# Performance work log

Hardware: AMD Instinct MI355X
Metric: run time of the kernel (lower is better)

The kernel has to match this reference:

```python
import jax, jax.numpy as jnp
import numpy as np

B, T, D = 2, 2048, 2048
H, KV, HD = 16, 8, 128
N_REP = H // KV
EPS = 1e-6
ROPE_THETA = 5e6
K_MASK = float(jnp.finfo(jnp.bfloat16).min)


def setup_inputs() -> dict:
    key = jax.random.key(0)
    ks = jax.random.split(key, 8)
    x = jax.random.normal(ks[0], (B, T, D), dtype=jnp.float32)
    wq = jax.random.normal(ks[1], (D, H * HD), dtype=jnp.float32) * 0.02
    wk = jax.random.normal(ks[2], (D, KV * HD), dtype=jnp.float32) * 0.02
    wv = jax.random.normal(ks[3], (D, KV * HD), dtype=jnp.float32) * 0.02
    wo = jax.random.normal(ks[4], (H * HD, D), dtype=jnp.float32) * 0.02
    qn_w = jnp.ones((HD,), dtype=jnp.float32)
    kn_w = jnp.ones((HD,), dtype=jnp.float32)
    # real rotary angles: [T, HD//2] -> broadcast to [B, T, HD//2]
    pos = jnp.arange(T, dtype=jnp.float32)
    inv_freq = 1.0 / (ROPE_THETA ** (jnp.arange(0, HD, 2, dtype=jnp.float32) / HD))
    ang = pos[:, None] * inv_freq[None, :]
    sin = jnp.broadcast_to(jnp.sin(ang)[None], (B, T, HD // 2))
    cos = jnp.broadcast_to(jnp.cos(ang)[None], (B, T, HD // 2))
    # causal mask [B, 1, T, T]
    causal = jnp.tril(jnp.ones((T, T), dtype=jnp.bool_))
    mask = jnp.broadcast_to(causal[None, None], (B, 1, T, T))
    k_cache = jnp.zeros((B, T, KV, HD), dtype=jnp.float32)
    v_cache = jnp.zeros((B, T, KV, HD), dtype=jnp.float32)
    return {"x": x, "wq": wq, "wk": wk, "wv": wv, "wo": wo,
            "qn_w": qn_w, "kn_w": kn_w, "sin": sin, "cos": cos,
            "mask": mask, "k_cache": k_cache, "v_cache": v_cache}


def _rms_norm(h, w):
    h32 = h.astype(jnp.float32)
    rms = jax.lax.rsqrt(jnp.mean(h32 * h32, axis=-1, keepdims=True) + EPS)
    return (h32 * rms * w).astype(h.dtype)


def _apply_rope(x, sin, cos):
    x1, x2 = x[..., : HD // 2], x[..., HD // 2:]
    s, c = sin[:, :, None, :], cos[:, :, None, :]  # [B,T,1,HD/2]
    return jnp.concatenate([x1 * c - x2 * s, x2 * c + x1 * s], axis=-1).astype(x.dtype)


def reference(x, wq, wk, wv, wo, qn_w, kn_w, sin, cos, mask, k_cache, v_cache):
    b, t, _ = x.shape
    q = _rms_norm((x @ wq).reshape(b, t, H, HD), qn_w)
    k = _rms_norm((x @ wk).reshape(b, t, KV, HD), kn_w)
    v = (x @ wv).reshape(b, t, KV, HD)
    q = _apply_rope(q, sin, cos)
    k = _apply_rope(k, sin, cos)
    # KV-cache update at cur_ind = 0 (prefill)
    k_cache = jax.lax.dynamic_update_slice(k_cache, k.astype(k_cache.dtype), (0, 0, 0, 0))
    v_cache = jax.lax.dynamic_update_slice(v_cache, v.astype(v_cache.dtype), (0, 0, 0, 0))
    # GQA repeat_kv: [B,S,KV,HD] -> [B,S,H,HD]
    kf = jnp.repeat(k_cache, N_REP, axis=2)
    vf = jnp.repeat(v_cache, N_REP, axis=2)
    scale = HD ** -0.5
    # [B,H,T,S]
    attn = jnp.einsum('bthd,bshd->bhts', q, kf) * scale
    attn = jnp.where(mask, attn, K_MASK)
    attn = jax.nn.softmax(attn.astype(jnp.float32), axis=-1).astype(q.dtype)
    out = jnp.einsum('bhts,bshd->bthd', attn, vf).reshape(b, t, H * HD)
    return out @ wo
```

## Files before the change

### kernel.cpp

```cpp
#include <hip/hip_runtime.h>
#include <hip/hip_bf16.h>
#include <stdint.h>

#define BB 2
#define TT 2048
#define DD 2048
#define HH 16
#define KVH 8
#define HDIM 128
#define BT (BB*TT)
#define NQKV (HH*HDIM + 2*KVH*HDIM)
#define TQ (TT/128)
#define ATT_SCALE 0.08838834764831845f
#define RMS_EPS 1e-6f

typedef __bf16 bf16;
typedef __bf16 bf16x8 __attribute__((ext_vector_type(8)));
typedef __bf16 bf16x4 __attribute__((ext_vector_type(4)));
typedef __bf16 bf16x2 __attribute__((ext_vector_type(2)));
typedef float  f32x4  __attribute__((ext_vector_type(4)));
typedef float  f32x16 __attribute__((ext_vector_type(16)));
typedef unsigned u32x4 __attribute__((ext_vector_type(4)));

__device__ __forceinline__ void gl_lds16(const void* g, const void* l) {
  __builtin_amdgcn_global_load_lds(
      (const __attribute__((address_space(1))) void*)(uintptr_t)g,
      (__attribute__((address_space(3))) void*)(uint32_t)(uintptr_t)l,
      16, 0, 0);
}

__device__ __forceinline__ unsigned pkbf(float lo, float hi) {
  bf16x2 t = { (bf16)lo, (bf16)hi };
  return __builtin_bit_cast(unsigned, t);
}

__global__ __launch_bounds__(256) void cast_bf16_k(const float* __restrict__ in,
                                                   bf16* __restrict__ out, int n4) {
  int i = blockIdx.x * blockDim.x + threadIdx.x;
  int stride = gridDim.x * blockDim.x;
  for (; i < n4; i += stride) {
    float4 v = ((const float4*)in)[i];
    bf16x4 o = { (bf16)v.x, (bf16)v.y, (bf16)v.z, (bf16)v.w };
    *(bf16x4*)(out + (size_t)i * 4) = o;
  }
}

__global__ __launch_bounds__(256) void transpose_cast_k(const float* __restrict__ in,
                                                        bf16* __restrict__ out,
                                                        int R, int C) {
  __shared__ float tile[32][33];
  int tx = threadIdx.x & 31, ty = threadIdx.x >> 5;
  int c0 = blockIdx.x * 32, r0 = blockIdx.y * 32;
#pragma unroll
  for (int i = 0; i < 4; ++i)
    tile[ty + 8*i][tx] = in[(size_t)(r0 + ty + 8*i) * C + c0 + tx];
  __syncthreads();
#pragma unroll
  for (int i = 0; i < 4; ++i)
    out[(size_t)(c0 + ty + 8*i) * R + r0 + tx] = (bf16)tile[tx][ty + 8*i];
}

__global__ __launch_bounds__(256) void transpose_v_k(const bf16* __restrict__ vb,
                                                     bf16* __restrict__ vbt) {
  __shared__ bf16 tile[32][33];
  int tx = threadIdx.x & 31, ty = threadIdx.x >> 5;
  int t0 = blockIdx.x * 32;
  int d0 = blockIdx.y * 32;
  int bk = blockIdx.z;
  int b = bk >> 3, kv = bk & 7;
#pragma unroll
  for (int i = 0; i < 4; ++i)
    tile[ty + 8*i][tx] = vb[(((size_t)(b*TT + t0 + ty + 8*i)) * KVH + kv) * HDIM + d0 + tx];
  __syncthreads();
#pragma unroll
  for (int i = 0; i < 4; ++i)
    vbt[(((size_t)bk) * HDIM + d0 + ty + 8*i) * TT + t0 + tx] = tile[tx][ty + 8*i];
}

template <int OUT_F32>
__global__ __launch_bounds__(512, 2)
void gemm256_k(const bf16* __restrict__ A, const bf16* __restrict__ Bt,
               void* __restrict__ Cout, int M, int N, int K) {
  __shared__ bf16 S[2 * 2 * 2 * 128 * 64];
  const int tid = threadIdx.x, lane = tid & 63, wid = tid >> 6;
  const int lr = lane & 15, lq = lane >> 4;
  const int wrow = wid >> 1, wcol = wid & 1;

  const int nwg = gridDim.x;
  const int o = blockIdx.x;
  const int ns = (o & 7) * (nwg >> 3) + (o >> 3);
  const int GX = N >> 8;
  const int by = ns / GX, bx = ns % GX;

  const int NT = K >> 6;
  const bf16* Ab = A + (size_t)(by * 256) * K;
  const bf16* Bb = Bt + (size_t)(bx * 256) * K;

  const int srow = tid >> 3;
  const size_t soff = (size_t)srow * K + (((tid & 7) ^ (srow & 7)) * 8);
  const int ldst0 = wid * 512;

  auto STAGE = [&](int op, int h, int t_) {
    int tc = t_ < NT ? t_ : NT - 1;
    const bf16* src = (op ? Bb : Ab) + soff + (size_t)(h * 128) * K + tc * 64;
    bf16* dst = S + ((((((t_ & 1) << 1) | op) << 1) | h) << 13) + ldst0;
#pragma unroll
    for (int i = 0; i < 2; ++i)
      gl_lds16(src + (size_t)(i * 64) * K, dst + i * 4096);
  };

  bf16x8 af[2][2][2];
  bf16x8 bfr[4][2];
  f32x4 acc[4][2][4] = {};

  auto LOAD_A = [&](int buf) {
#pragma unroll
    for (int mh = 0; mh < 2; ++mh) {
      const bf16* base = S + (((buf << 2) | mh) << 13);
#pragma unroll
      for (int m = 0; m < 2; ++m) {
        int ra = wrow * 32 + m * 16 + lr;
#pragma unroll
        for (int ks = 0; ks < 2; ++ks)
          af[mh][m][ks] = *(const bf16x8*)(base + ra * 64 + (((ks * 4 + lq) ^ (ra & 7)) * 8));
      }
    }
  };
  auto LOAD_B = [&](int buf, int nh) {
    const bf16* base = S + (((buf << 2) | 2 | nh) << 13);
#pragma unroll
    for (int n = 0; n < 4; ++n) {
      int rb = wcol * 64 + n * 16 + lr;
#pragma unroll
      for (int ks = 0; ks < 2; ++ks)
        bfr[n][ks] = *(const bf16x8*)(base + rb * 64 + (((ks * 4 + lq) ^ (rb & 7)) * 8));
    }
  };
  auto MFMA_Q = [&](int qd, int mh) {
#pragma unroll
    for (int m = 0; m < 2; ++m)
#pragma unroll
      for (int n = 0; n < 4; ++n)
#pragma unroll
        for (int ks = 0; ks < 2; ++ks)
          acc[qd][m][n] = __builtin_amdgcn_mfma_f32_16x16x32_bf16(
              af[mh][m][ks], bfr[n][ks], acc[qd][m][n], 0, 0, 0);
  };

  STAGE(0, 0, 0); STAGE(0, 1, 0); STAGE(1, 0, 0); STAGE(1, 1, 0);
  STAGE(0, 0, 1); STAGE(0, 1, 1); STAGE(1, 0, 1);
  asm volatile("s_waitcnt vmcnt(6)" ::: "memory");
  __builtin_amdgcn_sched_barrier(0);
  __builtin_amdgcn_s_barrier();

  for (int t = 0; t < NT; ++t) {
    const int buf = t & 1;
    LOAD_A(buf);
    LOAD_B(buf, 0);
    STAGE(1, 1, t + 1);
    __builtin_amdgcn_s_barrier();
    asm volatile("s_waitcnt lgkmcnt(0)" ::: "memory");
    __builtin_amdgcn_sched_barrier(0);
    __builtin_amdgcn_s_setprio(1);
    MFMA_Q(0, 0);
    __builtin_amdgcn_s_setprio(0);
    __builtin_amdgcn_sched_barrier(0);
    __builtin_amdgcn_s_barrier();
    STAGE(0, 0, t + 2);
    __builtin_amdgcn_s_barrier();
    __builtin_amdgcn_s_setprio(1);
    MFMA_Q(1, 1);
    __builtin_amdgcn_s_setprio(0);
    __builtin_amdgcn_sched_barrier(0);
    __builtin_amdgcn_s_barrier();
    LOAD_B(buf, 1);
    STAGE(0, 1, t + 2);
    __builtin_amdgcn_s_barrier();
    asm volatile("s_waitcnt lgkmcnt(0)" ::: "memory");
    __builtin_amdgcn_sched_barrier(0);
    __builtin_amdgcn_s_setprio(1);
    MFMA_Q(2, 1);
    __builtin_amdgcn_s_setprio(0);
    __builtin_amdgcn_sched_barrier(0);
    __builtin_amdgcn_s_barrier();
    STAGE(1, 0, t + 2);
    asm volatile("s_waitcnt vmcnt(6)" ::: "memory");
    __builtin_amdgcn_sched_barrier(0);
    __builtin_amdgcn_s_barrier();
    __builtin_amdgcn_s_setprio(1);
    MFMA_Q(3, 0);
    __builtin_amdgcn_s_setprio(0);
    __builtin_amdgcn_sched_barrier(0);
    __builtin_amdgcn_s_barrier();
  }

#pragma unroll
  for (int qd = 0; qd < 4; ++qd) {
    const int mh = (qd == 1 || qd == 2) ? 1 : 0;
    const int nh = (qd >= 2) ? 1 : 0;
#pragma unroll
    for (int m = 0; m < 2; ++m)
#pragma unroll
      for (int n = 0; n < 4; ++n)
#pragma unroll
        for (int j = 0; j < 4; ++j) {
          int row = by * 256 + mh * 128 + wrow * 32 + m * 16 + lq * 4 + j;
          int col = bx * 256 + nh * 128 + wcol * 64 + n * 16 + lr;
          if (OUT_F32) ((float*)Cout)[(size_t)row * N + col] = acc[qd][m][n][j];
          else         ((bf16*)Cout)[(size_t)row * N + col] = (bf16)acc[qd][m][n][j];
        }
  }
}

__global__ __launch_bounds__(256) void norm_rope_k(const bf16* __restrict__ qkv,
                                                   const float* __restrict__ qn_w,
                                                   const float* __restrict__ kn_w,
                                                   const float* __restrict__ sinb,
                                                   const float* __restrict__ cosb,
                                                   bf16* __restrict__ qro,
                                                   bf16* __restrict__ kro,
                                                   bf16* __restrict__ vo) {
  const int bt = blockIdx.x;
  const int tid = threadIdx.x, lane = tid & 63, wid = tid >> 6;
  const bf16* row = qkv + (size_t)bt * NQKV;
  const float sv = sinb[bt * 64 + lane];
  const float cv = cosb[bt * 64 + lane];
  for (int it = 0; it < 8; ++it) {
    int hv = it * 4 + wid;
    int off = (hv < 16) ? hv * 128 : (hv < 24) ? 2048 + (hv - 16) * 128 : 3072 + (hv - 24) * 128;
    float e0 = (float)row[off + lane];
    float e1 = (float)row[off + 64 + lane];
    if (hv >= 24) {
      bf16* dst = vo + (size_t)bt * (KVH * HDIM) + (hv - 24) * 128;
      dst[lane] = (bf16)e0;
      dst[64 + lane] = (bf16)e1;
    } else {
      float ss = e0 * e0 + e1 * e1;
#pragma unroll
      for (int o = 32; o >= 1; o >>= 1) ss += __shfl_xor(ss, o, 64);
      float rms = rsqrtf(ss * (1.0f / 128.0f) + RMS_EPS);
      const float* wn = (hv < 16) ? qn_w : kn_w;
      float n0 = e0 * rms * wn[lane];
      float n1 = e1 * rms * wn[lane + 64];
      float o0 = n0 * cv - n1 * sv;
      float o1 = n1 * cv + n0 * sv;
      if (hv < 16) {
        bf16* dst = qro + (size_t)bt * (HH * HDIM) + hv * 128;
        dst[lane] = (bf16)o0; dst[64 + lane] = (bf16)o1;
      } else {
        bf16* dst = kro + (size_t)bt * (KVH * HDIM) + (hv - 16) * 128;
        dst[lane] = (bf16)o0; dst[64 + lane] = (bf16)o1;
      }
    }
  }
}

__global__ __launch_bounds__(256, 2)
void attn5_k(const bf16* __restrict__ qr, const bf16* __restrict__ kr,
             const bf16* __restrict__ vbt, bf16* __restrict__ ao) {
  __shared__ bf16 Ks[2][64 * 128];
  __shared__ bf16 Vs[2][128 * 64];
  __shared__ float Al[4][32];
  const int tid = threadIdx.x, lane = tid & 63, wid = tid >> 6;
  const int l31 = lane & 31, hi = lane >> 5;
  const int h = blockIdx.y, b = blockIdx.z;
  const int qt = (b & 1) ? (TQ - 1 - blockIdx.x) : blockIdx.x;
  const int kvh = h >> 1;
  const int q0w = qt * 128 + wid * 32;
  const int qg = q0w + l31;
  const int nt = 2 * qt + 2;

  auto STAGE = [&](int bufi, int kt) {
#pragma unroll
    for (int i = 0; i < 4; ++i) {
      int u = i * 256 + tid;
      int krow = u >> 4, kcc = u & 15;
      gl_lds16(&kr[(((size_t)(b * TT + kt * 64 + krow)) * KVH + kvh) * HDIM + ((kcc ^ (krow & 15)) * 8)],
               &Ks[bufi][(i * 256 + wid * 64) * 8]);
      int vrow = u >> 3, vcc = u & 7;
      gl_lds16(&vbt[(((size_t)(b * KVH + kvh)) * HDIM + vrow) * TT + kt * 64 + ((vcc ^ (vrow & 7)) * 8)],
               &Vs[bufi][(i * 256 + wid * 64) * 8]);
    }
  };

  bf16x8 qf[8];
  const bf16* qrow = &qr[(((size_t)(b * TT + qg)) * HH + h) * HDIM];
#pragma unroll
  for (int ks = 0; ks < 8; ++ks)
    qf[ks] = *(const bf16x8*)(qrow + ks * 16 + hi * 8);

  f32x16 accO[4] = {};
  float m = -INFINITY, lsum = 0.f;

  int buf = 0;
  STAGE(0, 0);
  __syncthreads();

  for (int kt = 0; kt < nt; ++kt) {
    if (kt + 1 < nt) STAGE(buf ^ 1, kt + 1);

    if (kt * 64 <= q0w + 31) {
      const char* Kb = (const char*)&Ks[buf][0];
      const char* Vb = (const char*)&Vs[buf][0];

      f32x16 sacc[2];
#pragma unroll
      for (int ct = 0; ct < 2; ++ct) {
#pragma unroll
        for (int j = 0; j < 16; ++j) sacc[ct][j] = 0.f;
        int krow = ct * 32 + l31;
#pragma unroll
        for (int ks = 0; ks < 8; ++ks) {
          bf16x8 kf = *(const bf16x8*)(Kb + krow * 256 + (((2 * ks + hi) ^ (krow & 15)) * 16));
          sacc[ct] = __builtin_amdgcn_mfma_f32_32x32x16_bf16(kf, qf[ks], sacc[ct], 0, 0, 0);
        }
      }

      const bool domask = (kt * 64 + 63 > q0w);
      float p[2][16];
      float pmx = -INFINITY;
#pragma unroll
      for (int ct = 0; ct < 2; ++ct) {
        int lim = qg - (kt * 64 + ct * 32 + 4 * hi);
#pragma unroll
        for (int r = 0; r < 16; ++r) {
          const int crow0 = (r & 3) + 8 * (r >> 2);
          float v = sacc[ct][r] * ATT_SCALE;
          v = (!domask || crow0 <= lim) ? v : -INFINITY;
          p[ct][r] = v;
          pmx = fmaxf(pmx, v);
        }
      }
      pmx = fmaxf(pmx, __shfl_xor(pmx, 32, 64));

      if (__any(pmx > m + 8.f)) {
        float mnew = fmaxf(m, pmx);
        float alpha = __expf(m - mnew);
        m = mnew;
        lsum *= alpha;
        if (lane < 32) Al[wid][l31] = alpha;
        __builtin_amdgcn_s_waitcnt(0);
#pragma unroll
        for (int n = 0; n < 4; ++n)
#pragma unroll
          for (int r = 0; r < 16; ++r) {
            const int crow = (r & 3) + 8 * (r >> 2) + 4 * hi;
            accO[n][r] *= Al[wid][crow];
          }
      }

      float rsum = 0.f;
#pragma unroll
      for (int ct = 0; ct < 2; ++ct)
#pragma unroll
        for (int r = 0; r < 16; ++r) {
          float e = __expf(p[ct][r] - m);
          p[ct][r] = e;
          rsum += e;
        }
      rsum += __shfl_xor(rsum, 32, 64);
      lsum += rsum;

      bf16x8 pa[4];
#pragma unroll
      for (int ct = 0; ct < 2; ++ct) {
        unsigned W[8];
#pragma unroll
        for (int mi = 0; mi < 8; ++mi)
          W[mi] = pkbf(p[ct][2 * mi], p[ct][2 * mi + 1]);
#pragma unroll
        for (int a = 0; a < 2; ++a) {
          unsigned s0 = __shfl_xor(W[4 * a + 0], 32, 64);
          unsigned s1 = __shfl_xor(W[4 * a + 1], 32, 64);
          unsigned s2 = __shfl_xor(W[4 * a + 2], 32, 64);
          unsigned s3 = __shfl_xor(W[4 * a + 3], 32, 64);
          u32x4 wv;
          wv[0] = hi ? s2 : W[4 * a + 0];
          wv[1] = hi ? s3 : W[4 * a + 1];
          wv[2] = hi ? W[4 * a + 2] : s0;
          wv[3] = hi ? W[4 * a + 3] : s1;
          pa[ct * 2 + a] = __builtin_bit_cast(bf16x8, wv);
        }
      }

#pragma unroll
      for (int n = 0; n < 4; ++n) {
        int vrow = n * 32 + l31;
#pragma unroll
        for (int ks = 0; ks < 4; ++ks) {
          bf16x8 vf = *(const bf16x8*)(Vb + vrow * 128 + (((2 * ks + hi) ^ (vrow & 7)) * 16));
          accO[n] = __builtin_amdgcn_mfma_f32_32x32x16_bf16(pa[ks], vf, accO[n], 0, 0, 0);
        }
      }
    }

    __syncthreads();
    buf ^= 1;
  }

  float inv = 1.0f / lsum;
  __syncthreads();
  if (lane < 32) Al[wid][l31] = inv;
  __builtin_amdgcn_s_waitcnt(0);
#pragma unroll
  for (int n = 0; n < 4; ++n)
#pragma unroll
    for (int r = 0; r < 16; ++r) {
      const int crow = (r & 3) + 8 * (r >> 2) + 4 * hi;
      size_t idx = (((size_t)(b * TT + q0w + crow)) * HH + h) * HDIM + n * 32 + l31;
      ao[idx] = (bf16)(accO[n][r] * Al[wid][crow]);
    }
}

extern "C" void kernel_launch(void* const* d_in, const int* in_sizes, int n_in,
                              void* d_out, int out_size, void* d_ws, size_t ws_size,
                              hipStream_t stream) {
  const float* x    = (const float*)d_in[0];
  const float* wq   = (const float*)d_in[1];
  const float* wk   = (const float*)d_in[2];
  const float* wv   = (const float*)d_in[3];
  const float* wo   = (const float*)d_in[4];
  const float* qn_w = (const float*)d_in[5];
  const float* kn_w = (const float*)d_in[6];
  const float* sinb = (const float*)d_in[7];
  const float* cosb = (const float*)d_in[8];
  float* out = (float*)d_out;

  char* ws = (char*)d_ws;
  size_t off = 0;
  auto alloc = [&](size_t bytes) {
    char* p = ws + off;
    off += (bytes + 255) & ~(size_t)255;
    return p;
  };
  bf16* xb  = (bf16*)alloc((size_t)BT * DD * 2);
  bf16* Wt  = (bf16*)alloc((size_t)NQKV * DD * 2);
  bf16* Wot = (bf16*)alloc((size_t)DD * DD * 2);
  bf16* qkv = (bf16*)alloc((size_t)BT * NQKV * 2);
  bf16* kro = (bf16*)alloc((size_t)BT * KVH * HDIM * 2);
  bf16* vb  = (bf16*)alloc((size_t)BT * KVH * HDIM * 2);
  bf16* vbt = (bf16*)alloc((size_t)BT * KVH * HDIM * 2);
  bf16* qro = Wt;
  bf16* aob = xb;
  (void)ws_size; (void)in_sizes; (void)n_in; (void)out_size;

  cast_bf16_k<<<2048, 256, 0, stream>>>(x, xb, BT * DD / 4);
  transpose_cast_k<<<dim3(2048 / 32, 2048 / 32), 256, 0, stream>>>(wq, Wt, 2048, 2048);
  transpose_cast_k<<<dim3(1024 / 32, 2048 / 32), 256, 0, stream>>>(wk, Wt + (size_t)2048 * 2048, 2048, 1024);
  transpose_cast_k<<<dim3(1024 / 32, 2048 / 32), 256, 0, stream>>>(wv, Wt + (size_t)3072 * 2048, 2048, 1024);
  transpose_cast_k<<<dim3(2048 / 32, 2048 / 32), 256, 0, stream>>>(wo, Wot, 2048, 2048);

  gemm256_k<0><<<dim3((BT / 256) * (NQKV / 256)), 512, 0, stream>>>(xb, Wt, qkv, BT, NQKV, DD);

  norm_rope_k<<<BT, 256, 0, stream>>>(qkv, qn_w, kn_w, sinb, cosb, qro, kro, vb);
  transpose_v_k<<<dim3(TT / 32, HDIM / 32, BB * KVH), 256, 0, stream>>>(vb, vbt);

  attn5_k<<<dim3(TQ, HH, BB), 256, 0, stream>>>(qro, kro, vbt, aob);

  gemm256_k<1><<<dim3((BT / 256) * (DD / 256)), 512, 0, stream>>>(aob, Wot, out, BT, DD, DD);
}
```

Measured before the change: 231.5 us.

## Read K/V directly from global in attention, relayout K, use smaller output GEMM

Attention drops LDS staging and double buffering. Each wave now reads K and V fragments straight from global memory, using a new head-major K layout written by the norm/rope kernel. It also skips fully masked 32-key halves, walks only the tiles each wave needs, folds log2e into the scale so it can use exp2f, broadcasts rescale factors with ds_bpermute, and orders blocks so heads sharing a KV group are adjacent. The output projection switches from the 256-tile GEMM to a new, simpler 128x128 GEMM without double buffering. This removes LDS traffic and block-wide syncs, at the cost of uncached global loads and a possibly less efficient final GEMM.

```diff
diff --git a/kernel.cpp b/kernel.cpp
--- a/kernel.cpp
+++ b/kernel.cpp
@@ -78,6 +78,58 @@
 }
 
 template <int OUT_F32>
+__global__ __launch_bounds__(256, 2)
+void gemm_bt_k(const bf16* __restrict__ A, const bf16* __restrict__ Bt,
+               void* __restrict__ Cout, int M, int N, int K) {
+  __shared__ bf16 As[128 * 32];
+  __shared__ bf16 Bs[128 * 32];
+  const int tid = threadIdx.x;
+  const int lane = tid & 63, wid = tid >> 6;
+  const int lr = lane & 15, lq = lane >> 4;
+  const int bm = blockIdx.y * 128, bn = blockIdx.x * 128;
+  const int wr = wid >> 1, wc = wid & 1;
+  const bf16* Ab = A + (size_t)bm * K;
+  const bf16* Bb = Bt + (size_t)bn * K;
+  f32x4 acc[4][4] = {};
+  for (int k0 = 0; k0 < K; k0 += 32) {
+#pragma unroll
+    for (int r = 0; r < 2; ++r) {
+      int ch = r * 256 + tid;
+      int row = ch >> 2, c8 = ch & 3;
+      const bf16* lbase = As + (size_t)(r * 256 + wid * 64) * 8;
+      gl_lds16(Ab + (size_t)row * K + k0 + c8 * 8, lbase);
+      const bf16* lbase2 = Bs + (size_t)(r * 256 + wid * 64) * 8;
+      gl_lds16(Bb + (size_t)row * K + k0 + c8 * 8, lbase2);
+    }
+    __syncthreads();
+    bf16x8 af[4], bfv[4];
+#pragma unroll
+    for (int m = 0; m < 4; ++m)
+      af[m] = *(const bf16x8*)&As[(wr * 64 + m * 16 + lr) * 32 + lq * 8];
+#pragma unroll
+    for (int n = 0; n < 4; ++n)
+      bfv[n] = *(const bf16x8*)&Bs[(wc * 64 + n * 16 + lr) * 32 + lq * 8];
+#pragma unroll
+    for (int m = 0; m < 4; ++m)
+#pragma unroll
+      for (int n = 0; n < 4; ++n)
+        acc[m][n] = __builtin_amdgcn_mfma_f32_16x16x32_bf16(af[m], bfv[n], acc[m][n], 0, 0, 0);
+    __syncthreads();
+  }
+#pragma unroll
+  for (int m = 0; m < 4; ++m)
+#pragma unroll
+    for (int n = 0; n < 4; ++n)
+#pragma unroll
+      for (int r = 0; r < 4; ++r) {
+        int row = bm + wr * 64 + m * 16 + lq * 4 + r;
+        int col = bn + wc * 64 + n * 16 + lr;
+        if (OUT_F32) ((float*)Cout)[(size_t)row * N + col] = acc[m][n][r];
+        else         ((bf16*)Cout)[(size_t)row * N + col] = (bf16)acc[m][n][r];
+      }
+}
+
+template <int OUT_F32>
 __global__ __launch_bounds__(512, 2)
 void gemm256_k(const bf16* __restrict__ A, const bf16* __restrict__ Bt,
                void* __restrict__ Cout, int M, int N, int K) {
@@ -221,6 +273,7 @@
                                                    bf16* __restrict__ kro,
                                                    bf16* __restrict__ vo) {
   const int bt = blockIdx.x;
+  const int b = bt >> 11, t = bt & 2047;
   const int tid = threadIdx.x, lane = tid & 63, wid = tid >> 6;
   const bf16* row = qkv + (size_t)bt * NQKV;
   const float sv = sinb[bt * 64 + lane];
@@ -248,7 +301,7 @@
         bf16* dst = qro + (size_t)bt * (HH * HDIM) + hv * 128;
         dst[lane] = (bf16)o0; dst[64 + lane] = (bf16)o1;
       } else {
-        bf16* dst = kro + (size_t)bt * (KVH * HDIM) + (hv - 16) * 128;
+        bf16* dst = kro + (((size_t)b * KVH + (hv - 16)) * TT + t) * HDIM;
         dst[lane] = (bf16)o0; dst[64 + lane] = (bf16)o1;
       }
     }
@@ -256,32 +309,21 @@
 }
 
 __global__ __launch_bounds__(256, 2)
-void attn5_k(const bf16* __restrict__ qr, const bf16* __restrict__ kr,
+void attn6_k(const bf16* __restrict__ qr, const bf16* __restrict__ kr2,
              const bf16* __restrict__ vbt, bf16* __restrict__ ao) {
-  __shared__ bf16 Ks[2][64 * 128];
-  __shared__ bf16 Vs[2][128 * 64];
-  __shared__ float Al[4][32];
   const int tid = threadIdx.x, lane = tid & 63, wid = tid >> 6;
   const int l31 = lane & 31, hi = lane >> 5;
-  const int h = blockIdx.y, b = blockIdx.z;
-  const int qt = (b & 1) ? (TQ - 1 - blockIdx.x) : blockIdx.x;
-  const int kvh = h >> 1;
+  const int o = blockIdx.x;
+  const int c = o & 15, rr = o >> 4;
+  const int b = c >> 3, kvh = c & 7;
+  const int h = kvh * 2 + (rr & 1);
+  const int qtx = rr >> 1;
+  const int qt = b ? (TQ - 1 - qtx) : qtx;
   const int q0w = qt * 128 + wid * 32;
   const int qg = q0w + l31;
-  const int nt = 2 * qt + 2;
-
-  auto STAGE = [&](int bufi, int kt) {
-#pragma unroll
-    for (int i = 0; i < 4; ++i) {
-      int u = i * 256 + tid;
-      int krow = u >> 4, kcc = u & 15;
-      gl_lds16(&kr[(((size_t)(b * TT + kt * 64 + krow)) * KVH + kvh) * HDIM + ((kcc ^ (krow & 15)) * 8)],
-               &Ks[bufi][(i * 256 + wid * 64) * 8]);
-      int vrow = u >> 3, vcc = u & 7;
-      gl_lds16(&vbt[(((size_t)(b * KVH + kvh)) * HDIM + vrow) * TT + kt * 64 + ((vcc ^ (vrow & 7)) * 8)],
-               &Vs[bufi][(i * 256 + wid * 64) * 8]);
-    }
-  };
+
+  const bf16* Kbase = kr2 + ((size_t)(b * KVH + kvh)) * TT * HDIM;
+  const bf16* Vbase = vbt + ((size_t)(b * KVH + kvh)) * ((size_t)HDIM * TT);
 
   bf16x8 qf[8];
   const bf16* qrow = &qr[(((size_t)(b * TT + qg)) * HH + h) * HDIM];
@@ -291,79 +333,92 @@
 
   f32x16 accO[4] = {};
   float m = -INFINITY, lsum = 0.f;
-
-  int buf = 0;
-  STAGE(0, 0);
-  __syncthreads();
-
-  for (int kt = 0; kt < nt; ++kt) {
-    if (kt + 1 < nt) STAGE(buf ^ 1, kt + 1);
-
-    if (kt * 64 <= q0w + 31) {
-      const char* Kb = (const char*)&Ks[buf][0];
-      const char* Vb = (const char*)&Vs[buf][0];
-
-      f32x16 sacc[2];
+  const float SC2 = ATT_SCALE * 1.4426950408889634f;
+  const int ntw = (q0w >> 6) + 1;
+
+  for (int kt = 0; kt < ntw; ++kt) {
+    const bool do1 = (kt * 64 + 32) <= (q0w + 31);
+    const bool domask = (kt * 64 + 63) > q0w;
+
+    f32x16 sacc[2];
+#pragma unroll
+    for (int ct = 0; ct < 2; ++ct) {
+      if (ct == 0 || do1) {
+#pragma unroll
+        for (int j = 0; j < 16; ++j) sacc[ct][j] = 0.f;
+        const bf16* Krow = Kbase + (size_t)(kt * 64 + ct * 32 + l31) * HDIM + hi * 8;
+#pragma unroll
+        for (int ks = 0; ks < 8; ++ks) {
+          bf16x8 kf = *(const bf16x8*)(Krow + ks * 16);
+          sacc[ct] = __builtin_amdgcn_mfma_f32_32x32x16_bf16(kf, qf[ks], sacc[ct], 0, 0, 0);
+        }
+      }
+    }
+
+    float p[2][16];
+    float pmx = -INFINITY;
+    if (domask) {
 #pragma unroll
       for (int ct = 0; ct < 2; ++ct) {
-#pragma unroll
-        for (int j = 0; j < 16; ++j) sacc[ct][j] = 0.f;
-        int krow = ct * 32 + l31;
-#pragma unroll
-        for (int ks = 0; ks < 8; ++ks) {
-          bf16x8 kf = *(const bf16x8*)(Kb + krow * 256 + (((2 * ks + hi) ^ (krow & 15)) * 16));
-          sacc[ct] = __builtin_amdgcn_mfma_f32_32x32x16_bf16(kf, qf[ks], sacc[ct], 0, 0, 0);
-        }
-      }
-
-      const bool domask = (kt * 64 + 63 > q0w);
-      float p[2][16];
-      float pmx = -INFINITY;
+        if (ct == 0 || do1) {
+          int lim = qg - (kt * 64 + ct * 32 + 4 * hi);
+#pragma unroll
+          for (int r = 0; r < 16; ++r) {
+            const int crow0 = (r & 3) + 8 * (r >> 2);
+            float v = sacc[ct][r] * SC2;
+            v = (crow0 <= lim) ? v : -INFINITY;
+            p[ct][r] = v;
+            pmx = fmaxf(pmx, v);
+          }
+        }
+      }
+    } else {
 #pragma unroll
       for (int ct = 0; ct < 2; ++ct) {
-        int lim = qg - (kt * 64 + ct * 32 + 4 * hi);
+        if (ct == 0 || do1) {
+#pragma unroll
+          for (int r = 0; r < 16; ++r) {
+            float v = sacc[ct][r] * SC2;
+            p[ct][r] = v;
+            pmx = fmaxf(pmx, v);
+          }
+        }
+      }
+    }
+    pmx = fmaxf(pmx, __shfl_xor(pmx, 32, 64));
+
+    if (__any(pmx > m + 11.54f)) {
+      float mnew = fmaxf(m, pmx);
+      float alpha = exp2f(m - mnew);
+      m = mnew;
+      lsum *= alpha;
+      int ai = __builtin_bit_cast(int, alpha);
+#pragma unroll
+      for (int r = 0; r < 16; ++r) {
+        const int crow = (r & 3) + 8 * (r >> 2) + 4 * hi;
+        float av = __builtin_bit_cast(float, __builtin_amdgcn_ds_bpermute(crow << 2, ai));
+#pragma unroll
+        for (int n = 0; n < 4; ++n) accO[n][r] *= av;
+      }
+    }
+
+    float rsum = 0.f;
+#pragma unroll
+    for (int ct = 0; ct < 2; ++ct)
+      if (ct == 0 || do1)
 #pragma unroll
         for (int r = 0; r < 16; ++r) {
-          const int crow0 = (r & 3) + 8 * (r >> 2);
-          float v = sacc[ct][r] * ATT_SCALE;
-          v = (!domask || crow0 <= lim) ? v : -INFINITY;
-          p[ct][r] = v;
-          pmx = fmaxf(pmx, v);
-        }
-      }
-      pmx = fmaxf(pmx, __shfl_xor(pmx, 32, 64));
-
-      if (__any(pmx > m + 8.f)) {
-        float mnew = fmaxf(m, pmx);
-        float alpha = __expf(m - mnew);
-        m = mnew;
-        lsum *= alpha;
-        if (lane < 32) Al[wid][l31] = alpha;
-        __builtin_amdgcn_s_waitcnt(0);
-#pragma unroll
-        for (int n = 0; n < 4; ++n)
-#pragma unroll
-          for (int r = 0; r < 16; ++r) {
-            const int crow = (r & 3) + 8 * (r >> 2) + 4 * hi;
-            accO[n][r] *= Al[wid][crow];
-          }
-      }
-
-      float rsum = 0.f;
-#pragma unroll
-      for (int ct = 0; ct < 2; ++ct)
-#pragma unroll
-        for (int r = 0; r < 16; ++r) {
-          float e = __expf(p[ct][r] - m);
+          float e = exp2f(p[ct][r] - m);
           p[ct][r] = e;
           rsum += e;
         }
-      rsum += __shfl_xor(rsum, 32, 64);
-      lsum += rsum;
-
-      bf16x8 pa[4];
-#pragma unroll
-      for (int ct = 0; ct < 2; ++ct) {
+    rsum += __shfl_xor(rsum, 32, 64);
+    lsum += rsum;
+
+    bf16x8 pa[4];
+#pragma unroll
+    for (int ct = 0; ct < 2; ++ct) {
+      if (ct == 0 || do1) {
         unsigned W[8];
 #pragma unroll
         for (int mi = 0; mi < 8; ++mi)
@@ -382,33 +437,36 @@
           pa[ct * 2 + a] = __builtin_bit_cast(bf16x8, wv);
         }
       }
-
-#pragma unroll
-      for (int n = 0; n < 4; ++n) {
-        int vrow = n * 32 + l31;
-#pragma unroll
-        for (int ks = 0; ks < 4; ++ks) {
-          bf16x8 vf = *(const bf16x8*)(Vb + vrow * 128 + (((2 * ks + hi) ^ (vrow & 7)) * 16));
+    }
+
+#pragma unroll
+    for (int n = 0; n < 4; ++n) {
+      const bf16* Vrow = Vbase + (size_t)(n * 32 + l31) * TT + kt * 64 + hi * 8;
+#pragma unroll
+      for (int ks = 0; ks < 4; ++ks) {
+        if (ks < 2 || do1) {
+          bf16x8 vf = *(const bf16x8*)(Vrow + ks * 16);
           accO[n] = __builtin_amdgcn_mfma_f32_32x32x16_bf16(pa[ks], vf, accO[n], 0, 0, 0);
         }
       }
     }
-
-    __syncthreads();
-    buf ^= 1;
   }
 
   float inv = 1.0f / lsum;
-  __syncthreads();
-  if (lane < 32) Al[wid][l31] = inv;
-  __builtin_amdgcn_s_waitcnt(0);
+  int ii = __builtin_bit_cast(int, inv);
+  float av[16];
+#pragma unroll
+  for (int r = 0; r < 16; ++r) {
+    const int crow = (r & 3) + 8 * (r >> 2) + 4 * hi;
+    av[r] = __builtin_bit_cast(float, __builtin_amdgcn_ds_bpermute(crow << 2, ii));
+  }
 #pragma unroll
   for (int n = 0; n < 4; ++n)
 #pragma unroll
     for (int r = 0; r < 16; ++r) {
       const int crow = (r & 3) + 8 * (r >> 2) + 4 * hi;
       size_t idx = (((size_t)(b * TT + q0w + crow)) * HH + h) * HDIM + n * 32 + l31;
-      ao[idx] = (bf16)(accO[n][r] * Al[wid][crow]);
+      ao[idx] = (bf16)(accO[n][r] * av[r]);
     }
 }
 
@@ -455,7 +513,7 @@
   norm_rope_k<<<BT, 256, 0, stream>>>(qkv, qn_w, kn_w, sinb, cosb, qro, kro, vb);
   transpose_v_k<<<dim3(TT / 32, HDIM / 32, BB * KVH), 256, 0, stream>>>(vb, vbt);
 
-  attn5_k<<<dim3(TQ, HH, BB), 256, 0, stream>>>(qro, kro, vbt, aob);
-
-  gemm256_k<1><<<dim3((BT / 256) * (DD / 256)), 512, 0, stream>>>(aob, Wot, out, BT, DD, DD);
-}
+  attn6_k<<<dim3(512), 256, 0, stream>>>(qro, kro, vbt, aob);
+
+  gemm_bt_k<1><<<dim3(DD / 128, BT / 128), 256, 0, stream>>>(aob, Wot, out, BT, DD, DD);
+}
```

Measured after the change: 342.8 us. 1.48x slower.
